# Optimization experiments

Measured on AMD Instinct MI355X. Metric: run time of the kernel, lower is better.

## Reference

```python
import jax, jax.numpy as jnp
import numpy as np

B, T, D = 64, 1024, 256


def setup_inputs() -> dict:
    key = jax.random.key(0)
    k0, k1, k2, k3, k4 = jax.random.split(key, 5)
    scale = 1.0 / np.sqrt(D)
    return {
        "s0": jax.random.normal(k0, (B, D), dtype=jnp.float32),
        "x": jax.random.normal(k1, (B, T, D), dtype=jnp.float32),
        "W": jax.random.normal(k2, (D, D), dtype=jnp.float32) * scale,
        "U": jax.random.normal(k3, (D, D), dtype=jnp.float32) * scale,
        "b": jax.random.normal(k4, (D,), dtype=jnp.float32),
    }


def reference(s0, x, W, U, b):
    """ONNX Scan v8 with one state var, one scan input (direction=0),
    one scan output, and outer vals (W, U, b).
    Body: new_state = tanh(state @ W + x_t @ U + b); scan_out = new_state.
    The Python batch loop in the original is embarrassingly parallel, so it is
    vectorized: the carried state is [B, D] and lax.scan runs over time.
    Returns (final_state [B, D], scan_output [B, T, D]).
    """

    def step(state, x_t):  # state: [B, D], x_t: [B, D]
        new_state = jnp.tanh(state @ W + x_t @ U + b)
        return new_state, new_state

    x_tbd = jnp.swapaxes(x, 0, 1)  # [T, B, D]
    final_state, ys = jax.lax.scan(step, s0, x_tbd)
    scan_out = jnp.swapaxes(ys, 0, 1)  # [B, T, D]
    return final_state, scan_out
```

## Files before the change

kernel.cpp:

```cpp
#include <hip/hip_runtime.h>
#include <math.h>

#define TDIM 1024
#define DDIM 256
#define BDIM 64

__global__ __launch_bounds__(256)
void xu_gemm(const float* __restrict__ x, const float* __restrict__ U,
             const float* __restrict__ bias, float* __restrict__ P)
{
    __shared__ float As[32][64];
    __shared__ float Bs[32][256];
    const int tid = threadIdx.x;
    const int tr = tid >> 5;
    const int tc = tid & 31;
    const long rowBase = (long)blockIdx.x * 64;

    float acc[8][8];
#pragma unroll
    for (int r = 0; r < 8; ++r)
#pragma unroll
        for (int c = 0; c < 8; ++c) acc[r][c] = 0.f;

    for (int k0 = 0; k0 < 256; k0 += 32) {
#pragma unroll
        for (int s = 0; s < 2; ++s) {
            int idx = tid * 2 + s;
            int r   = idx >> 3;
            int kq  = idx & 7;
            float4 v = *(const float4*)&x[(rowBase + r) * 256 + k0 + kq * 4];
            As[kq*4+0][r] = v.x;
            As[kq*4+1][r] = v.y;
            As[kq*4+2][r] = v.z;
            As[kq*4+3][r] = v.w;
        }
#pragma unroll
        for (int s = 0; s < 8; ++s) {
            int idx = tid + s * 256;
            int kk  = idx >> 6;
            int c4  = idx & 63;
            *(float4*)&Bs[kk][c4*4] = *(const float4*)&U[(k0 + kk) * 256 + c4*4];
        }
        __syncthreads();
#pragma unroll
        for (int kk = 0; kk < 32; ++kk) {
            float4 a0 = *(const float4*)&As[kk][tr*4];
            float4 a1 = *(const float4*)&As[kk][tr*4 + 32];
            float4 b0 = *(const float4*)&Bs[kk][tc*4];
            float4 b1 = *(const float4*)&Bs[kk][tc*4 + 128];
            float av[8] = {a0.x,a0.y,a0.z,a0.w,a1.x,a1.y,a1.z,a1.w};
            float bv[8] = {b0.x,b0.y,b0.z,b0.w,b1.x,b1.y,b1.z,b1.w};
#pragma unroll
            for (int r = 0; r < 8; ++r)
#pragma unroll
                for (int c = 0; c < 8; ++c)
                    acc[r][c] = fmaf(av[r], bv[c], acc[r][c]);
        }
        __syncthreads();
    }
    float4 bb0 = *(const float4*)&bias[tc*4];
    float4 bb1 = *(const float4*)&bias[tc*4 + 128];
#pragma unroll
    for (int r = 0; r < 8; ++r) {
        long row = rowBase + (r < 4 ? (tr*4 + r) : (32 + tr*4 + (r - 4)));
        float4 lo = make_float4(acc[r][0] + bb0.x, acc[r][1] + bb0.y,
                                acc[r][2] + bb0.z, acc[r][3] + bb0.w);
        float4 hi = make_float4(acc[r][4] + bb1.x, acc[r][5] + bb1.y,
                                acc[r][6] + bb1.z, acc[r][7] + bb1.w);
        *(float4*)&P[row * 256 + tc*4]       = lo;
        *(float4*)&P[row * 256 + tc*4 + 128] = hi;
    }
}

__global__ __launch_bounds__(1024)
void rnn_scan(const float* __restrict__ s0, const float* __restrict__ W,
              float* __restrict__ out)
{
    __shared__ float  s[256];
    __shared__ float2 red2[8][128];
    __shared__ float  pbuf[2][256];

    const int tid = threadIdx.x;
    const int q   = tid >> 7;
    const int jp  = tid & 127;
    const int row = blockIdx.x;
    const int j0  = jp * 2;

    float2 w[32];
#pragma unroll
    for (int i = 0; i < 32; ++i)
        w[i] = *(const float2*)&W[(q*32 + i) * 256 + j0];

    float* scanP = out + BDIM * DDIM + (long)row * TDIM * DDIM;

    if (tid < 64) {
        ((float4*)s)[tid]       = ((const float4*)(s0 + row * 256))[tid];
        ((float4*)pbuf[0])[tid] = ((const float4*)scanP)[tid];
    }
    __syncthreads();

    const float4* s4 = (const float4*)s;
    float4 pf;
    for (int t = 0; t < TDIM; ++t) {
        if (tid < 64) {
            int tn = (t + 1 < TDIM) ? t + 1 : TDIM - 1;
            pf = ((const float4*)(scanP + (long)tn * DDIM))[tid];
        }
        float2 acc = make_float2(0.f, 0.f);
#pragma unroll
        for (int i8 = 0; i8 < 8; ++i8) {
            float4 sv = s4[q * 8 + i8];
            float sk[4] = {sv.x, sv.y, sv.z, sv.w};
#pragma unroll
            for (int u = 0; u < 4; ++u) {
                acc.x = fmaf(sk[u], w[i8*4 + u].x, acc.x);
                acc.y = fmaf(sk[u], w[i8*4 + u].y, acc.y);
            }
        }
        red2[q][jp] = acc;
        __syncthreads();

        if (tid < 256) {
            const float* redf = (const float*)red2;
            float z = pbuf[t & 1][tid];
#pragma unroll
            for (int qq = 0; qq < 8; ++qq) z += redf[qq * 256 + tid];
            float h = 1.f - 2.f / (1.f + __expf(2.f * z));
            s[tid] = h;
            scanP[(long)t * DDIM + tid] = h;
            if (t == TDIM - 1) out[row * DDIM + tid] = h;
        }
        if (tid < 64) {
            ((float4*)pbuf[(t + 1) & 1])[tid] = pf;
        }
        __syncthreads();
    }
}

extern "C" void kernel_launch(void* const* d_in, const int* in_sizes, int n_in,
                              void* d_out, int out_size, void* d_ws, size_t ws_size,
                              hipStream_t stream) {
    (void)in_sizes; (void)n_in; (void)out_size; (void)d_ws; (void)ws_size;
    const float* s0 = (const float*)d_in[0];
    const float* x  = (const float*)d_in[1];
    const float* W  = (const float*)d_in[2];
    const float* U  = (const float*)d_in[3];
    const float* b  = (const float*)d_in[4];
    float* out = (float*)d_out;
    float* P   = out + BDIM * DDIM;

    xu_gemm<<<dim3(65536 / 64), dim3(256), 0, stream>>>(x, U, b, P);
    rnn_scan<<<dim3(BDIM), dim3(1024), 0, stream>>>(s0, W, out);
}
```

Before: 820.8 us.

## Use warp-shuffle reduction and double-buffered state in RNN scan; prefetch GEMM tiles

The recurrent scan kernel now assigns 8 adjacent lanes per output pair and reduces the partial dot products with xor shuffles, replacing the shared-memory reduction. With ping-pong state buffers each timestep needs one barrier instead of two, and the hidden state for step t is written to global memory one step late. The next P values are preloaded into registers two steps ahead. The xu GEMM also loads the next k-tile into registers while the current tile is being computed. The cost is higher register pressure and a more complex scheme of reading scanP ahead while overwriting it in place with delayed writes.

```diff
diff --git a/kernel.cpp b/kernel.cpp
--- a/kernel.cpp
+++ b/kernel.cpp
@@ -5,12 +5,18 @@
 #define DDIM 256
 #define BDIM 64
 
-__global__ __launch_bounds__(256)
+typedef float f32x2 __attribute__((ext_vector_type(2)));
+
+__device__ __forceinline__ float tanh_fast(float z) {
+    return 1.f - 2.f / (1.f + __expf(2.f * z));
+}
+
+__global__ __launch_bounds__(256, 3)
 void xu_gemm(const float* __restrict__ x, const float* __restrict__ U,
              const float* __restrict__ bias, float* __restrict__ P)
 {
-    __shared__ float As[32][64];
-    __shared__ float Bs[32][256];
+    __shared__ __align__(16) float As[32][64];
+    __shared__ __align__(16) float Bs[32][256];
     const int tid = threadIdx.x;
     const int tr = tid >> 5;
     const int tc = tid & 31;
@@ -22,26 +28,30 @@
 #pragma unroll
         for (int c = 0; c < 8; ++c) acc[r][c] = 0.f;
 
+    float4 xs[2], us[8];
+#define LOADX(K0) _Pragma("unroll") \
+    for (int s_ = 0; s_ < 2; ++s_) { int idx = tid*2+s_; int r_ = idx>>3; int kq = idx&7; \
+        xs[s_] = *(const float4*)&x[(rowBase + r_)*256 + (K0) + kq*4]; }
+#define LOADU(K0) _Pragma("unroll") \
+    for (int s_ = 0; s_ < 8; ++s_) { int idx = tid + s_*256; int kk_ = idx>>6; int c4 = idx&63; \
+        us[s_] = *(const float4*)&U[((K0)+kk_)*256 + c4*4]; }
+
+    LOADX(0); LOADU(0);
+
     for (int k0 = 0; k0 < 256; k0 += 32) {
 #pragma unroll
-        for (int s = 0; s < 2; ++s) {
-            int idx = tid * 2 + s;
-            int r   = idx >> 3;
-            int kq  = idx & 7;
-            float4 v = *(const float4*)&x[(rowBase + r) * 256 + k0 + kq * 4];
-            As[kq*4+0][r] = v.x;
-            As[kq*4+1][r] = v.y;
-            As[kq*4+2][r] = v.z;
-            As[kq*4+3][r] = v.w;
+        for (int s_ = 0; s_ < 2; ++s_) {
+            int idx = tid*2+s_; int r_ = idx>>3; int kq = idx&7;
+            As[kq*4+0][r_] = xs[s_].x; As[kq*4+1][r_] = xs[s_].y;
+            As[kq*4+2][r_] = xs[s_].z; As[kq*4+3][r_] = xs[s_].w;
         }
 #pragma unroll
-        for (int s = 0; s < 8; ++s) {
-            int idx = tid + s * 256;
-            int kk  = idx >> 6;
-            int c4  = idx & 63;
-            *(float4*)&Bs[kk][c4*4] = *(const float4*)&U[(k0 + kk) * 256 + c4*4];
+        for (int s_ = 0; s_ < 8; ++s_) {
+            int idx = tid + s_*256; int kk_ = idx>>6; int c4 = idx&63;
+            *(float4*)&Bs[kk_][c4*4] = us[s_];
         }
         __syncthreads();
+        if (k0 < 224) { LOADX(k0 + 32); LOADU(k0 + 32); }
 #pragma unroll
         for (int kk = 0; kk < 32; ++kk) {
             float4 a0 = *(const float4*)&As[kk][tr*4];
@@ -58,6 +68,7 @@
         }
         __syncthreads();
     }
+
     float4 bb0 = *(const float4*)&bias[tc*4];
     float4 bb1 = *(const float4*)&bias[tc*4 + 128];
 #pragma unroll
@@ -72,68 +83,77 @@
     }
 }
 
-__global__ __launch_bounds__(1024)
+__global__ __launch_bounds__(1024, 4)
 void rnn_scan(const float* __restrict__ s0, const float* __restrict__ W,
               float* __restrict__ out)
 {
-    __shared__ float  s[256];
-    __shared__ float2 red2[8][128];
-    __shared__ float  pbuf[2][256];
+    __shared__ __align__(16) float sb0[256];
+    __shared__ __align__(16) float sb1[256];
 
     const int tid = threadIdx.x;
-    const int q   = tid >> 7;
-    const int jp  = tid & 127;
+    const int jp  = tid >> 3;
+    const int q   = tid & 7;
     const int row = blockIdx.x;
-    const int j0  = jp * 2;
 
-    float2 w[32];
+    f32x2 w2[32];
 #pragma unroll
-    for (int i = 0; i < 32; ++i)
-        w[i] = *(const float2*)&W[(q*32 + i) * 256 + j0];
+    for (int i = 0; i < 8; ++i) {
+        int c = (i + q) & 7;
+#pragma unroll
+        for (int u = 0; u < 4; ++u)
+            w2[4*i+u] = *(const f32x2*)&W[(q*32 + c*4 + u) * 256 + 2*jp];
+    }
 
     float* scanP = out + BDIM * DDIM + (long)row * TDIM * DDIM;
 
-    if (tid < 64) {
-        ((float4*)s)[tid]       = ((const float4*)(s0 + row * 256))[tid];
-        ((float4*)pbuf[0])[tid] = ((const float4*)scanP)[tid];
-    }
+    f32x2 pa = *(const f32x2*)&scanP[2*jp];
+    f32x2 pb = *(const f32x2*)&scanP[256 + 2*jp];
+
+    if (tid < 64)
+        ((float4*)sb0)[tid] = ((const float4*)(s0 + row * 256))[tid];
     __syncthreads();
 
-    const float4* s4 = (const float4*)s;
-    float4 pf;
-    for (int t = 0; t < TDIM; ++t) {
-        if (tid < 64) {
-            int tn = (t + 1 < TDIM) ? t + 1 : TDIM - 1;
-            pf = ((const float4*)(scanP + (long)tn * DDIM))[tid];
-        }
-        float2 acc = make_float2(0.f, 0.f);
-#pragma unroll
-        for (int i8 = 0; i8 < 8; ++i8) {
-            float4 sv = s4[q * 8 + i8];
-            float sk[4] = {sv.x, sv.y, sv.z, sv.w};
-#pragma unroll
-            for (int u = 0; u < 4; ++u) {
-                acc.x = fmaf(sk[u], w[i8*4 + u].x, acc.x);
-                acc.y = fmaf(sk[u], w[i8*4 + u].y, acc.y);
-            }
-        }
-        red2[q][jp] = acc;
-        __syncthreads();
+#define BODY(T, SIN, SOUT, PREG)                                              \
+  {                                                                           \
+    if ((T) > 0 && (tid & 63) < 4) {         \
+        int fi = ((tid >> 6) << 2) + (tid & 63);                              \
+        float4 h4 = ((const float4*)(SIN))[fi];                               \
+        *(float4*)&scanP[(long)((T) - 1) * 256 + fi * 4] = h4;                \
+    }                                                                         \
+    const float4* s4p = (const float4*)(SIN);                                 \
+    f32x2 a0 = {0.f, 0.f}, a1 = {0.f, 0.f};                                   \
+    _Pragma("unroll")                                                         \
+    for (int i = 0; i < 8; ++i) {                                             \
+        float4 sv = s4p[q * 8 + ((i + q) & 7)];      \
+        a0 += w2[4*i]     * sv.x;                                             \
+        a1 += w2[4*i + 1] * sv.y;                                             \
+        a0 += w2[4*i + 2] * sv.z;                                             \
+        a1 += w2[4*i + 3] * sv.w;                                             \
+    }                                                                         \
+    f32x2 accv = a0 + a1;                                                     \
+    float zx = accv.x, zy = accv.y;                                           \
+    zx += __shfl_xor(zx, 1); zy += __shfl_xor(zy, 1);                         \
+    zx += __shfl_xor(zx, 2); zy += __shfl_xor(zy, 2);                         \
+    zx += __shfl_xor(zx, 4); zy += __shfl_xor(zy, 4);                         \
+    zx += (PREG).x; zy += (PREG).y;                                           \
+    float hx = tanh_fast(zx), hy = tanh_fast(zy);                             \
+    if (q == 0) { f32x2 h2; h2.x = hx; h2.y = hy;                             \
+                  *(f32x2*)&(SOUT)[2*jp] = h2; }                              \
+    __syncthreads();                                                          \
+  }
 
-        if (tid < 256) {
-            const float* redf = (const float*)red2;
-            float z = pbuf[t & 1][tid];
-#pragma unroll
-            for (int qq = 0; qq < 8; ++qq) z += redf[qq * 256 + tid];
-            float h = 1.f - 2.f / (1.f + __expf(2.f * z));
-            s[tid] = h;
-            scanP[(long)t * DDIM + tid] = h;
-            if (t == TDIM - 1) out[row * DDIM + tid] = h;
-        }
-        if (tid < 64) {
-            ((float4*)pbuf[(t + 1) & 1])[tid] = pf;
-        }
-        __syncthreads();
+    for (int t = 0; t < TDIM; t += 2) {
+        f32x2 pnA = *(const f32x2*)&scanP[(long)((t + 2) & 1023) * 256 + 2*jp];
+        f32x2 pnB = *(const f32x2*)&scanP[(long)((t + 3) & 1023) * 256 + 2*jp];
+        BODY(t,     sb0, sb1, pa);
+        BODY(t + 1, sb1, sb0, pb);
+        pa = pnA; pb = pnB;
+    }
+
+    if (tid < 64) {
+        float4 h4 = ((const float4*)sb0)[tid];
+        *(float4*)&scanP[(long)(TDIM - 1) * 256 + tid * 4] = h4;
+        *(float4*)&out[row * 256 + tid * 4] = h4;
     }
 }
 
```

Result: slower. 1.263 ms (+53.9%).
